# Kernel tuning notes

Measured on AMD Instinct MI355X. Metric: run time of the kernel, lower is better.

## Reference

```python
import jax, jax.numpy as jnp
import numpy as np

B, D, H, NB = 4096, 2048, 2048, 4
BIN, BOUT = D // NB, H // NB
EPS = 1e-5


def _block_linear(x, W, b):
    # x: [B, nb*bin], W: [nb, bin, bout], b: [nb, bout] -> [B, nb*bout]
    xr = x.reshape(x.shape[0], NB, BIN)
    y = jnp.einsum('bni,nio->bno', xr, W) + b
    return y.reshape(x.shape[0], NB * BOUT)


def setup_inputs() -> dict:
    key = jax.random.key(0)
    ks = jax.random.split(key, 24)
    sW = 1.0 / np.sqrt(BIN)
    sR = 1.0 / np.sqrt(BOUT)
    inp = {
        'x': jax.random.normal(ks[0], (B, D), jnp.float32),
        'h_prev': jax.random.normal(ks[1], (B, H), jnp.float32),
        'c_prev': jax.random.normal(ks[2], (B, H), jnp.float32),
        'ln_g': jnp.ones((D,), jnp.float32),
        'ln_b': jnp.zeros((D,), jnp.float32),
        'conv_w': jax.random.normal(ks[3], (3,), jnp.float32) * 0.5,
        'conv_b': jnp.zeros((), jnp.float32),
    }
    names = ['Wz', 'Wi', 'Wf', 'Wo']
    for j, n in enumerate(names):
        inp[n] = jax.random.normal(ks[4 + j], (NB, BIN, BOUT), jnp.float32) * sW
        inp['b' + n[1]] = jax.random.normal(ks[8 + j], (NB, BOUT), jnp.float32) * sW
    rnames = ['Rz', 'Ri', 'Rf', 'Ro']
    for j, n in enumerate(rnames):
        inp[n] = jax.random.normal(ks[12 + j], (NB, BOUT, BOUT), jnp.float32) * sR
        inp['rb' + n[1]] = jax.random.normal(ks[16 + j], (NB, BOUT), jnp.float32) * sR
    return inp


def reference(x, h_prev, c_prev, ln_g, ln_b, conv_w, conv_b,
              Wz, bz, Wi, bi, Wf, bf, Wo, bo,
              Rz, rbz, Ri, rbi, Rf, rbf, Ro, rbo):
    # LayerNorm over the feature dim
    mu = jnp.mean(x, axis=-1, keepdims=True)
    var = jnp.mean((x - mu) ** 2, axis=-1, keepdims=True)
    x_norm = (x - mu) * jax.lax.rsqrt(var + EPS) * ln_g + ln_b

    # Causal conv1d (kernel 3) along the feature axis, then SiLU
    xp = jnp.pad(x_norm, ((0, 0), (2, 0)))  # left-pad 2 -> causal
    xc = conv_w[0] * xp[:, :D] + conv_w[1] * xp[:, 1:D + 1] + conv_w[2] * xp[:, 2:D + 2] + conv_b
    x_conv = jax.nn.silu(xc)

    z = jnp.tanh(_block_linear(x, Wz, bz) + _block_linear(h_prev, Rz, rbz))
    i = jax.nn.sigmoid(_block_linear(x_conv, Wi, bi) + _block_linear(h_prev, Ri, rbi))
    f = jax.nn.sigmoid(_block_linear(x_conv, Wf, bf) + _block_linear(h_prev, Rf, rbf))
    o = jax.nn.sigmoid(_block_linear(x, Wo, bo) + _block_linear(h_prev, Ro, rbo))

    c_t = f * c_prev + i * z
    h_t = o * jnp.tanh(c_t)
    return (h_t, c_t)
```

## Files before the change

### kernel.cpp

```cpp
#include <hip/hip_runtime.h>
#include <hip/hip_bf16.h>
#include <math.h>

#define BB 4096
#define DD 2048
#define HH 2048

typedef __bf16 bf16x8 __attribute__((ext_vector_type(8)));
typedef float f32x4 __attribute__((ext_vector_type(4)));

__device__ __forceinline__ void async16(const void* g, void* l) {
  __builtin_amdgcn_global_load_lds(
      (const __attribute__((address_space(1))) unsigned int*)g,
      (__attribute__((address_space(3))) unsigned int*)l,
      16, 0, 0);
}

template <int N>
__device__ __forceinline__ void wait_vmcnt() {
  asm volatile("s_waitcnt vmcnt(%0)" ::"n"(N) : "memory");
}

__device__ __forceinline__ float sigmoidf_(float x) {
  return 1.0f / (1.0f + __expf(-x));
}
__device__ __forceinline__ float tanhf_(float x) {
  float t = __expf(-2.0f * fabsf(x));
  return copysignf((1.0f - t) / (1.0f + t), x);
}

__device__ __forceinline__ void store_bf8(__hip_bfloat16* dst, const float* v) {
  union { __hip_bfloat16 b[8]; uint4 u; } p;
#pragma unroll
  for (int e = 0; e < 8; e++) p.b[e] = __float2bfloat16(v[e]);
  *(uint4*)dst = p.u;
}

__global__ __launch_bounds__(256) void prep_all(
    const float* __restrict__ x, const float* __restrict__ h,
    const float* __restrict__ lg, const float* __restrict__ lb,
    const float* __restrict__ cw, const float* __restrict__ cb,
    __hip_bfloat16* __restrict__ xh2, __hip_bfloat16* __restrict__ xc2,
    const float* __restrict__ Wz, const float* __restrict__ Wi,
    const float* __restrict__ Wf, const float* __restrict__ Wo,
    const float* __restrict__ Rz, const float* __restrict__ Ri,
    const float* __restrict__ Rf, const float* __restrict__ Ro,
    __hip_bfloat16* __restrict__ WT2,
    const float* __restrict__ bz, const float* __restrict__ bi,
    const float* __restrict__ bf, const float* __restrict__ bo,
    const float* __restrict__ rbz, const float* __restrict__ rbi,
    const float* __restrict__ rbf, const float* __restrict__ rbo,
    float* __restrict__ bias) {
  __shared__ float smf[4224];
  const int b = blockIdx.x, t = threadIdx.x;

  if (b < 4096) {
    const int r = b, l = t & 63;
    const int mb = r >> 7, rl = r & 127, swz = (rl >> 1) & 3;
    const int n = t >> 6, ktl = (t >> 2) & 15, pc = (t & 3) ^ swz;
    float* red = smf;
    float* edge = smf + 8;
    const float* xr = x + (size_t)r * 2048;
    const float* hr = h + (size_t)r * 2048;
    float4 v0 = ((const float4*)xr)[t * 2];
    float4 v1 = ((const float4*)xr)[t * 2 + 1];
    float vv[8] = {v0.x, v0.y, v0.z, v0.w, v1.x, v1.y, v1.z, v1.w};
    float s = 0.f, s2 = 0.f;
#pragma unroll
    for (int e = 0; e < 8; e++) { s += vv[e]; s2 += vv[e] * vv[e]; }
#pragma unroll
    for (int off = 32; off > 0; off >>= 1) {
      s += __shfl_down(s, off);
      s2 += __shfl_down(s2, off);
    }
    const int w = t >> 6;
    if (l == 0) { red[w] = s; red[4 + w] = s2; }
    __syncthreads();
    const float mu = (red[0] + red[1] + red[2] + red[3]) * (1.0f / 2048.0f);
    const float var = (red[4] + red[5] + red[6] + red[7]) * (1.0f / 2048.0f) - mu * mu;
    const float rs = rsqrtf(var + 1e-5f);

    float4 h0 = ((const float4*)hr)[t * 2];
    float4 h1 = ((const float4*)hr)[t * 2 + 1];
    float hh[8] = {h0.x, h0.y, h0.z, h0.w, h1.x, h1.y, h1.z, h1.w};
    float4 g0 = ((const float4*)lg)[t * 2], g1 = ((const float4*)lg)[t * 2 + 1];
    float4 b0 = ((const float4*)lb)[t * 2], b1 = ((const float4*)lb)[t * 2 + 1];
    float gg[8] = {g0.x, g0.y, g0.z, g0.w, g1.x, g1.y, g1.z, g1.w};
    float bbv[8] = {b0.x, b0.y, b0.z, b0.w, b1.x, b1.y, b1.z, b1.w};
    float fr[8];
#pragma unroll
    for (int e = 0; e < 8; e++) fr[e] = (vv[e] - mu) * rs * gg[e] + bbv[e];

    const size_t bx = ((size_t)(mb * 4 + n) * 32 + ktl) * 512 + rl * 4 + pc;
    const size_t bh = ((size_t)(mb * 4 + n) * 32 + 16 + ktl) * 512 + rl * 4 + pc;
    store_bf8(xh2 + bx * 8, vv);
    store_bf8(xh2 + bh * 8, hh);

    edge[t * 2 + 0] = fr[6]; edge[t * 2 + 1] = fr[7];
    __syncthreads();
    float p6 = __shfl_up(fr[6], 1);
    float p7 = __shfl_up(fr[7], 1);
    if (l == 0) {
      p6 = (t > 0) ? edge[(t - 1) * 2 + 0] : 0.f;
      p7 = (t > 0) ? edge[(t - 1) * 2 + 1] : 0.f;
    }
    const float w0 = cw[0], w1 = cw[1], w2 = cw[2], cbv = cb[0];
    float sc[8];
    {
      float xc0 = w0 * p6 + w1 * p7 + w2 * fr[0] + cbv;
      float xc1 = w0 * p7 + w1 * fr[0] + w2 * fr[1] + cbv;
      sc[0] = xc0 * sigmoidf_(xc0);
      sc[1] = xc1 * sigmoidf_(xc1);
    }
#pragma unroll
    for (int e = 2; e < 8; e++) {
      float xc = w0 * fr[e - 2] + w1 * fr[e - 1] + w2 * fr[e] + cbv;
      sc[e] = xc * sigmoidf_(xc);
    }
    const size_t bc = ((size_t)(mb * 4 + n) * 16 + ktl) * 512 + rl * 4 + pc;
    store_bf8(xc2 + bc * 8, sc);

  } else if (b < 6144) {
    const int flat = b - 4096;
    const int jt = flat & 15;
    const int ksg = (flat >> 4) & 7;
    const int gn = flat >> 7;
    const int g = gn >> 2, nn = gn & 3;
    const float* src;
    if (ksg < 4) src = (g == 0 ? Wz : g == 1 ? Wi : g == 2 ? Wf : Wo);
    else         src = (g == 0 ? Rz : g == 1 ? Ri : g == 2 ? Rf : Ro);
    const int kb = (ksg & 3) * 128;

    {
      const int r8 = t >> 3, c4 = t & 7;
      const float* sp = src + ((size_t)nn * 512 + kb + r8) * 512 + jt * 32 + c4 * 4;
#pragma unroll
      for (int rr = 0; rr < 4; rr++) {
        float4 v = *(const float4*)(sp + (size_t)rr * 32 * 512);
        float* d = smf + (r8 + rr * 32) * 33 + c4 * 4;
        d[0] = v.x; d[1] = v.y; d[2] = v.z; d[3] = v.w;
      }
    }
    __syncthreads();
#pragma unroll
    for (int q = 0; q < 2; q++) {
      int u = t + q * 256;
      int ksl = u >> 7, j = (u >> 2) & 31, pc = u & 3;
      int c = pc ^ ((j >> 1) & 3);
      int krl = ksl * 32 + c * 8;
      float v[8];
#pragma unroll
      for (int e = 0; e < 8; e++) v[e] = smf[(krl + e) * 33 + j];
      size_t gr = ((size_t)(gn * 16 + jt) * 32 + ksg * 4 + ksl) * 128 + j * 4 + pc;
      store_bf8(WT2 + gr * 8, v);
    }

  } else {
    int i = (b - 6144) * 256 + t;
    if (i < 2048) {
      bias[0 * 2048 + i] = bz[i] + rbz[i];
      bias[1 * 2048 + i] = bi[i] + rbi[i];
      bias[2 * 2048 + i] = bf[i] + rbf[i];
      bias[3 * 2048 + i] = bo[i] + rbo[i];
    }
  }
}

__global__ __launch_bounds__(512, 4) void gemm_fused(
    const __hip_bfloat16* __restrict__ xh2, const __hip_bfloat16* __restrict__ xc2,
    const __hip_bfloat16* __restrict__ WT2, const float* __restrict__ bias,
    const float* __restrict__ c_prev, float* __restrict__ out) {
  __shared__ __attribute__((aligned(16))) char smem[65536];
  __hip_bfloat16* zo = (__hip_bfloat16*)smem;

  const int mb = blockIdx.x, jt = blockIdx.y, n = blockIdx.z;
  const int t = threadIdx.x, w = t >> 6, l = t & 63;
  const int pair = w >> 2, mhalf = (w >> 1) & 1, jhalf = w & 1;
  const int lj = l & 15;

  const char* gAu = (const char*)xh2 + (size_t)(mb * 4 + n) * 262144;
  const char* gCu = (const char*)xc2 + (size_t)(mb * 4 + n) * 131072;
  const char* gBu = (const char*)WT2 + (size_t)(n * 16 + jt * 2) * 65536;

  const int tA = t * 16;
  const int bg0 = t >> 8, bj0 = (t >> 7) & 1, br0 = t & 127;
  const int u1 = t + 512;
  const int bg1 = u1 >> 8, bj1 = (u1 >> 7) & 1, br1 = u1 & 127;
  const int vB0 = (bg0 * 64 + bj0) * 65536 + br0 * 16;
  const int vB1 = (bg1 * 64 + bj1) * 65536 + br1 * 16;
  const int dB0 = 16384 + bg0 * 4096 + bj0 * 2048 + br0 * 16;
  const int dB1 = 16384 + bg1 * 4096 + bj1 * 2048 + br1 * 16;

  const int fo = lj * 64 + (((l >> 4) ^ ((lj >> 1) & 3)) * 16);
  const int g0 = pair ? 1 : 0, g1 = pair ? 2 : 3;

  f32x4 acc[4][2][2] = {};

#define BAR() __builtin_amdgcn_s_barrier()
#define SBZ() __builtin_amdgcn_sched_barrier(0)

#define STAGE(H)                                                               \
  do {                                                                         \
    async16(gAu + ((H) * 8192 + 0) + tA, smem + ((H) & 1) * 32768 + tA);       \
    if ((H) < 16)                                                              \
      async16(gCu + ((H) * 8192) + tA, smem + ((H) & 1) * 32768 + 8192 + tA);  \
    async16(gBu + ((H) * 2048) + vB0, smem + ((H) & 1) * 32768 + dB0);         \
    async16(gBu + ((H) * 2048) + vB1, smem + ((H) & 1) * 32768 + dB1);         \
  } while (0)

#define MFMA8(sj, B0, B1)                                                      \
  do {                                                                         \
    acc[0][sj][0] = __builtin_amdgcn_mfma_f32_16x16x32_bf16(af0, B0, acc[0][sj][0], 0, 0, 0); \
    acc[1][sj][0] = __builtin_amdgcn_mfma_f32_16x16x32_bf16(af1, B0, acc[1][sj][0], 0, 0, 0); \
    acc[2][sj][0] = __builtin_amdgcn_mfma_f32_16x16x32_bf16(af2, B0, acc[2][sj][0], 0, 0, 0); \
    acc[3][sj][0] = __builtin_amdgcn_mfma_f32_16x16x32_bf16(af3, B0, acc[3][sj][0], 0, 0, 0); \
    acc[0][sj][1] = __builtin_amdgcn_mfma_f32_16x16x32_bf16(af0, B1, acc[0][sj][1], 0, 0, 0); \
    acc[1][sj][1] = __builtin_amdgcn_mfma_f32_16x16x32_bf16(af1, B1, acc[1][sj][1], 0, 0, 0); \
    acc[2][sj][1] = __builtin_amdgcn_mfma_f32_16x16x32_bf16(af2, B1, acc[2][sj][1], 0, 0, 0); \
    acc[3][sj][1] = __builtin_amdgcn_mfma_f32_16x16x32_bf16(af3, B1, acc[3][sj][1], 0, 0, 0); \
  } while (0)

#define STEP(KS)                                                               \
  do {                                                                         \
    if ((KS) < 31) STAGE((KS) + 1);                                            \
    wait_vmcnt<((KS) + 1 < 16) ? 4 : (((KS) + 1 < 32) ? 3 : 0)>();             \
    BAR(); SBZ();                                                              \
    const char* Ab = smem + ((KS) & 1) * 32768 +                               \
                     (((KS) < 16 && pair) ? 8192 : 0) + mhalf * 4096 + fo;     \
    const char* Bb = smem + ((KS) & 1) * 32768 + 16384 + jhalf * 2048 + fo;    \
    bf16x8 af0 = *(const bf16x8*)(Ab);                                         \
    bf16x8 af1 = *(const bf16x8*)(Ab + 1024);                                  \
    bf16x8 af2 = *(const bf16x8*)(Ab + 2048);                                  \
    bf16x8 af3 = *(const bf16x8*)(Ab + 3072);                                  \
    bf16x8 b00 = *(const bf16x8*)(Bb + g0 * 4096);                             \
    bf16x8 b10 = *(const bf16x8*)(Bb + g1 * 4096);                             \
    bf16x8 b01 = *(const bf16x8*)(Bb + g0 * 4096 + 1024);                      \
    bf16x8 b11 = *(const bf16x8*)(Bb + g1 * 4096 + 1024);                      \
    SBZ();                                                                     \
    __builtin_amdgcn_s_setprio(1);                                             \
    MFMA8(0, b00, b10);                                                        \
    MFMA8(1, b01, b11);                                                        \
    __builtin_amdgcn_s_setprio(0);                                             \
    SBZ(); BAR();                                                              \
  } while (0)

  STAGE(0);

  STEP(0);  STEP(1);  STEP(2);  STEP(3);
  STEP(4);  STEP(5);  STEP(6);  STEP(7);
  STEP(8);  STEP(9);  STEP(10); STEP(11);
  STEP(12); STEP(13); STEP(14); STEP(15);
  STEP(16); STEP(17); STEP(18); STEP(19);
  STEP(20); STEP(21); STEP(22); STEP(23);
  STEP(24); STEP(25); STEP(26); STEP(27);
  STEP(28); STEP(29); STEP(30); STEP(31);

  const int r0 = (l >> 4) * 4;
  const int colb = n * 512 + jt * 64;
  __syncthreads();
  if (pair == 0) {
#pragma unroll
    for (int sj = 0; sj < 2; ++sj) {
      const int jc = jhalf * 32 + sj * 16 + lj;
      const float bz_ = bias[colb + jc];
      const float bo_ = bias[3 * 2048 + colb + jc];
#pragma unroll
      for (int s = 0; s < 4; ++s) {
#pragma unroll
        for (int rr = 0; rr < 4; ++rr) {
          const int rl = mhalf * 64 + s * 16 + r0 + rr;
          zo[rl * 72 + jc] = __float2bfloat16(tanhf_(acc[s][sj][0][rr] + bz_));
          zo[(128 + rl) * 72 + jc] = __float2bfloat16(sigmoidf_(acc[s][sj][1][rr] + bo_));
        }
      }
    }
  }
  __syncthreads();
  if (pair == 1) {
    const size_t HC = (size_t)BB * HH;
#pragma unroll
    for (int sj = 0; sj < 2; ++sj) {
      const int jc = jhalf * 32 + sj * 16 + lj;
      const int col = colb + jc;
      const float bi_ = bias[1 * 2048 + col];
      const float bf_ = bias[2 * 2048 + col];
#pragma unroll
      for (int s = 0; s < 4; ++s) {
#pragma unroll
        for (int rr = 0; rr < 4; ++rr) {
          const int rl = mhalf * 64 + s * 16 + r0 + rr;
          const int row = mb * 128 + rl;
          const float z  = __bfloat162float(zo[rl * 72 + jc]);
          const float og = __bfloat162float(zo[(128 + rl) * 72 + jc]);
          const float ig = sigmoidf_(acc[s][sj][0][rr] + bi_);
          const float fg = sigmoidf_(acc[s][sj][1][rr] + bf_);
          const float cp = c_prev[(size_t)row * 2048 + col];
          const float c = fg * cp + ig * z;
          const float hv = og * tanhf_(c);
          out[(size_t)row * 2048 + col] = hv;
          out[HC + (size_t)row * 2048 + col] = c;
        }
      }
    }
  }
}

extern "C" void kernel_launch(void* const* d_in, const int* in_sizes, int n_in,
                              void* d_out, int out_size, void* d_ws, size_t ws_size,
                              hipStream_t stream) {
  const float* x      = (const float*)d_in[0];
  const float* h_prev = (const float*)d_in[1];
  const float* c_prev = (const float*)d_in[2];
  const float* ln_g   = (const float*)d_in[3];
  const float* ln_b   = (const float*)d_in[4];
  const float* conv_w = (const float*)d_in[5];
  const float* conv_b = (const float*)d_in[6];
  const float* Wz = (const float*)d_in[7];
  const float* bz = (const float*)d_in[8];
  const float* Wi = (const float*)d_in[9];
  const float* bi = (const float*)d_in[10];
  const float* Wf = (const float*)d_in[11];
  const float* bf = (const float*)d_in[12];
  const float* Wo = (const float*)d_in[13];
  const float* bo = (const float*)d_in[14];
  const float* Rz = (const float*)d_in[15];
  const float* rbz = (const float*)d_in[16];
  const float* Ri = (const float*)d_in[17];
  const float* rbi = (const float*)d_in[18];
  const float* Rf = (const float*)d_in[19];
  const float* rbf = (const float*)d_in[20];
  const float* Ro = (const float*)d_in[21];
  const float* rbo = (const float*)d_in[22];
  float* out = (float*)d_out;

  char* ws = (char*)d_ws;
  __hip_bfloat16* xh2 = (__hip_bfloat16*)(ws);
  __hip_bfloat16* xc2 = (__hip_bfloat16*)(ws + 33554432);
  __hip_bfloat16* WT2 = (__hip_bfloat16*)(ws + 33554432 + 16777216);
  float* bias         = (float*)(ws + 33554432 + 2 * 16777216);

  prep_all<<<6152, 256, 0, stream>>>(
      x, h_prev, ln_g, ln_b, conv_w, conv_b, xh2, xc2,
      Wz, Wi, Wf, Wo, Rz, Ri, Rf, Ro, WT2,
      bz, bi, bf, bo, rbz, rbi, rbf, rbo, bias);
  gemm_fused<<<dim3(32, 8, 4), 512, 0, stream>>>(xh2, xc2, WT2, bias, c_prev, out);
}
```

Before: 322.3 us.

## Split activation prep into row-per-wave kernel with LDS-staged coalesced stores

```diff
diff --git a/kernel.cpp b/kernel.cpp
--- a/kernel.cpp
+++ b/kernel.cpp
@@ -36,11 +36,123 @@
   *(uint4*)dst = p.u;
 }
 
-__global__ __launch_bounds__(256) void prep_all(
+__device__ __forceinline__ void st_bf4_lds(__hip_bfloat16* p, const float* v) {
+  union { __hip_bfloat16 b[4]; uint2 u; } t;
+#pragma unroll
+  for (int e = 0; e < 4; e++) t.b[e] = __float2bfloat16(v[e]);
+  *(uint2*)p = t.u;
+}
+
+#define ROWP 2056
+__global__ __launch_bounds__(512, 2) void prep_act(
     const float* __restrict__ x, const float* __restrict__ h,
     const float* __restrict__ lg, const float* __restrict__ lb,
     const float* __restrict__ cw, const float* __restrict__ cb,
-    __hip_bfloat16* __restrict__ xh2, __hip_bfloat16* __restrict__ xc2,
+    __hip_bfloat16* __restrict__ xh2, __hip_bfloat16* __restrict__ xc2) {
+  __shared__ __attribute__((aligned(16))) __hip_bfloat16 tile[8 * ROWP];
+  const int t = threadIdx.x, w = t >> 6, l = t & 63;
+  const int r0 = blockIdx.x * 8;
+  const int mb = r0 >> 7, rl0 = r0 & 127;
+  const int r = r0 + w;
+
+  const float* xr = x + (size_t)r * 2048;
+  const float* hr = h + (size_t)r * 2048;
+
+  float xv[32], hv[32];
+#pragma unroll
+  for (int q = 0; q < 8; q++) {
+    float4 v = ((const float4*)xr)[l + q * 64];
+    xv[q * 4 + 0] = v.x; xv[q * 4 + 1] = v.y; xv[q * 4 + 2] = v.z; xv[q * 4 + 3] = v.w;
+  }
+#pragma unroll
+  for (int q = 0; q < 8; q++) {
+    float4 v = ((const float4*)hr)[l + q * 64];
+    hv[q * 4 + 0] = v.x; hv[q * 4 + 1] = v.y; hv[q * 4 + 2] = v.z; hv[q * 4 + 3] = v.w;
+  }
+
+  float s = 0.f, s2 = 0.f;
+#pragma unroll
+  for (int e = 0; e < 32; e++) { s += xv[e]; s2 += xv[e] * xv[e]; }
+#pragma unroll
+  for (int off = 32; off > 0; off >>= 1) {
+    s += __shfl_xor(s, off);
+    s2 += __shfl_xor(s2, off);
+  }
+  const float mu = s * (1.0f / 2048.0f);
+  const float var = s2 * (1.0f / 2048.0f) - mu * mu;
+  const float rs = rsqrtf(var + 1e-5f);
+
+#define FLUSH(PART)                                                            \
+  do {                                                                         \
+    _Pragma("unroll")                                                          \
+    for (int k = 0; k < 4; ++k) {                                              \
+      const int gi = k * 512 + t;                                              \
+      const int pc = gi & 3, rr = (gi >> 2) & 7, grp = gi >> 5;                \
+      const int n_ = grp >> 4, ktl_ = grp & 15;                                \
+      const int c_ = pc ^ (((rl0 + rr) >> 1) & 3);                             \
+      bf16x8 v = *(const bf16x8*)(tile + rr * ROWP + n_ * 512 + ktl_ * 32 + c_ * 8); \
+      size_t G;                                                                \
+      if ((PART) == 2)                                                         \
+        G = ((size_t)(mb * 4 + n_) * 16 + ktl_) * 512 + (rl0 + rr) * 4 + pc;   \
+      else                                                                     \
+        G = ((size_t)(mb * 4 + n_) * 32 + ((PART) ? 16 : 0) + ktl_) * 512 +    \
+            (rl0 + rr) * 4 + pc;                                               \
+      *(bf16x8*)(((PART) == 2 ? xc2 : xh2) + G * 8) = v;                       \
+    }                                                                          \
+  } while (0)
+
+#pragma unroll
+  for (int q = 0; q < 8; q++)
+    st_bf4_lds(tile + w * ROWP + q * 256 + l * 4, &xv[q * 4]);
+  __syncthreads();
+  FLUSH(0);
+  __syncthreads();
+
+#pragma unroll
+  for (int q = 0; q < 8; q++)
+    st_bf4_lds(tile + w * ROWP + q * 256 + l * 4, &hv[q * 4]);
+  __syncthreads();
+  FLUSH(1);
+  __syncthreads();
+
+  float fr[32];
+#pragma unroll
+  for (int q = 0; q < 8; q++) {
+    float4 gv = ((const float4*)lg)[l + q * 64];
+    float4 bv = ((const float4*)lb)[l + q * 64];
+    fr[q * 4 + 0] = (xv[q * 4 + 0] - mu) * rs * gv.x + bv.x;
+    fr[q * 4 + 1] = (xv[q * 4 + 1] - mu) * rs * gv.y + bv.y;
+    fr[q * 4 + 2] = (xv[q * 4 + 2] - mu) * rs * gv.z + bv.z;
+    fr[q * 4 + 3] = (xv[q * 4 + 3] - mu) * rs * gv.w + bv.w;
+  }
+
+  const float w0 = cw[0], w1 = cw[1], w2 = cw[2], cbv = cb[0];
+  float c1 = 0.f, c2 = 0.f;
+#pragma unroll
+  for (int q = 0; q < 8; q++) {
+    float pm1 = __shfl_up(fr[q * 4 + 3], 1);
+    float pm2 = __shfl_up(fr[q * 4 + 2], 1);
+    if (l == 0) { pm1 = c1; pm2 = c2; }
+    float sc[4];
+    {
+      float v0 = w0 * pm2 + w1 * pm1 + w2 * fr[q * 4 + 0] + cbv;
+      float v1 = w0 * pm1 + w1 * fr[q * 4 + 0] + w2 * fr[q * 4 + 1] + cbv;
+      float v2 = w0 * fr[q * 4 + 0] + w1 * fr[q * 4 + 1] + w2 * fr[q * 4 + 2] + cbv;
+      float v3 = w0 * fr[q * 4 + 1] + w1 * fr[q * 4 + 2] + w2 * fr[q * 4 + 3] + cbv;
+      sc[0] = v0 * sigmoidf_(v0);
+      sc[1] = v1 * sigmoidf_(v1);
+      sc[2] = v2 * sigmoidf_(v2);
+      sc[3] = v3 * sigmoidf_(v3);
+    }
+    c1 = __shfl(fr[q * 4 + 3], 63);
+    c2 = __shfl(fr[q * 4 + 2], 63);
+    st_bf4_lds(tile + w * ROWP + q * 256 + l * 4, sc);
+  }
+  __syncthreads();
+  FLUSH(2);
+}
+
+__global__ __launch_bounds__(256) void prep_wb(
     const float* __restrict__ Wz, const float* __restrict__ Wi,
     const float* __restrict__ Wf, const float* __restrict__ Wo,
     const float* __restrict__ Rz, const float* __restrict__ Ri,
@@ -54,77 +166,10 @@
   __shared__ float smf[4224];
   const int b = blockIdx.x, t = threadIdx.x;
 
-  if (b < 4096) {
-    const int r = b, l = t & 63;
-    const int mb = r >> 7, rl = r & 127, swz = (rl >> 1) & 3;
-    const int n = t >> 6, ktl = (t >> 2) & 15, pc = (t & 3) ^ swz;
-    float* red = smf;
-    float* edge = smf + 8;
-    const float* xr = x + (size_t)r * 2048;
-    const float* hr = h + (size_t)r * 2048;
-    float4 v0 = ((const float4*)xr)[t * 2];
-    float4 v1 = ((const float4*)xr)[t * 2 + 1];
-    float vv[8] = {v0.x, v0.y, v0.z, v0.w, v1.x, v1.y, v1.z, v1.w};
-    float s = 0.f, s2 = 0.f;
-#pragma unroll
-    for (int e = 0; e < 8; e++) { s += vv[e]; s2 += vv[e] * vv[e]; }
-#pragma unroll
-    for (int off = 32; off > 0; off >>= 1) {
-      s += __shfl_down(s, off);
-      s2 += __shfl_down(s2, off);
-    }
-    const int w = t >> 6;
-    if (l == 0) { red[w] = s; red[4 + w] = s2; }
-    __syncthreads();
-    const float mu = (red[0] + red[1] + red[2] + red[3]) * (1.0f / 2048.0f);
-    const float var = (red[4] + red[5] + red[6] + red[7]) * (1.0f / 2048.0f) - mu * mu;
-    const float rs = rsqrtf(var + 1e-5f);
-
-    float4 h0 = ((const float4*)hr)[t * 2];
-    float4 h1 = ((const float4*)hr)[t * 2 + 1];
-    float hh[8] = {h0.x, h0.y, h0.z, h0.w, h1.x, h1.y, h1.z, h1.w};
-    float4 g0 = ((const float4*)lg)[t * 2], g1 = ((const float4*)lg)[t * 2 + 1];
-    float4 b0 = ((const float4*)lb)[t * 2], b1 = ((const float4*)lb)[t * 2 + 1];
-    float gg[8] = {g0.x, g0.y, g0.z, g0.w, g1.x, g1.y, g1.z, g1.w};
-    float bbv[8] = {b0.x, b0.y, b0.z, b0.w, b1.x, b1.y, b1.z, b1.w};
-    float fr[8];
-#pragma unroll
-    for (int e = 0; e < 8; e++) fr[e] = (vv[e] - mu) * rs * gg[e] + bbv[e];
-
-    const size_t bx = ((size_t)(mb * 4 + n) * 32 + ktl) * 512 + rl * 4 + pc;
-    const size_t bh = ((size_t)(mb * 4 + n) * 32 + 16 + ktl) * 512 + rl * 4 + pc;
-    store_bf8(xh2 + bx * 8, vv);
-    store_bf8(xh2 + bh * 8, hh);
-
-    edge[t * 2 + 0] = fr[6]; edge[t * 2 + 1] = fr[7];
-    __syncthreads();
-    float p6 = __shfl_up(fr[6], 1);
-    float p7 = __shfl_up(fr[7], 1);
-    if (l == 0) {
-      p6 = (t > 0) ? edge[(t - 1) * 2 + 0] : 0.f;
-      p7 = (t > 0) ? edge[(t - 1) * 2 + 1] : 0.f;
-    }
-    const float w0 = cw[0], w1 = cw[1], w2 = cw[2], cbv = cb[0];
-    float sc[8];
-    {
-      float xc0 = w0 * p6 + w1 * p7 + w2 * fr[0] + cbv;
-      float xc1 = w0 * p7 + w1 * fr[0] + w2 * fr[1] + cbv;
-      sc[0] = xc0 * sigmoidf_(xc0);
-      sc[1] = xc1 * sigmoidf_(xc1);
-    }
-#pragma unroll
-    for (int e = 2; e < 8; e++) {
-      float xc = w0 * fr[e - 2] + w1 * fr[e - 1] + w2 * fr[e] + cbv;
-      sc[e] = xc * sigmoidf_(xc);
-    }
-    const size_t bc = ((size_t)(mb * 4 + n) * 16 + ktl) * 512 + rl * 4 + pc;
-    store_bf8(xc2 + bc * 8, sc);
-
-  } else if (b < 6144) {
-    const int flat = b - 4096;
-    const int jt = flat & 15;
-    const int ksg = (flat >> 4) & 7;
-    const int gn = flat >> 7;
+  if (b < 2048) {
+    const int jt = b & 15;
+    const int ksg = (b >> 4) & 7;
+    const int gn = b >> 7;
     const int g = gn >> 2, nn = gn & 3;
     const float* src;
     if (ksg < 4) src = (g == 0 ? Wz : g == 1 ? Wi : g == 2 ? Wf : Wo);
@@ -156,7 +201,7 @@
     }
 
   } else {
-    int i = (b - 6144) * 256 + t;
+    int i = (b - 2048) * 256 + t;
     if (i < 2048) {
       bias[0 * 2048 + i] = bz[i] + rbz[i];
       bias[1 * 2048 + i] = bi[i] + rbi[i];
@@ -339,9 +384,10 @@
   __hip_bfloat16* WT2 = (__hip_bfloat16*)(ws + 33554432 + 16777216);
   float* bias         = (float*)(ws + 33554432 + 2 * 16777216);
 
-  prep_all<<<6152, 256, 0, stream>>>(
-      x, h_prev, ln_g, ln_b, conv_w, conv_b, xh2, xc2,
+  prep_wb<<<2056, 256, 0, stream>>>(
       Wz, Wi, Wf, Wo, Rz, Ri, Rf, Ro, WT2,
       bz, bi, bf, bo, rbz, rbi, rbf, rbo, bias);
+  prep_act<<<512, 512, 0, stream>>>(
+      x, h_prev, ln_g, ln_b, conv_w, conv_b, xh2, xc2);
   gemm_fused<<<dim3(32, 8, 4), 512, 0, stream>>>(xh2, xc2, WT2, bias, c_prev, out);
 }
```

Result: no change. 328.2 us (+1.8%).
